# Performance work log

Measured on AMD Instinct MI355X. Metric: run time of the kernel, lower is better.

## Reference

```python
import jax, jax.numpy as jnp
import numpy as np

B, CIN, COUT, H, W, K = 32, 256, 256, 56, 56, 3
STRIDE, PAD, DIL = 1, 1, 1
SPARSITY = 0.9  # fraction of weight entries pruned to zero


def setup_inputs() -> dict:
    key = jax.random.key(0)
    kx, kw, km = jax.random.split(key, 3)
    x = jax.random.normal(kx, (B, CIN, H, W), dtype=jnp.float32)
    w = jax.random.normal(kw, (COUT, CIN, K, K), dtype=jnp.float32)
    mask = (jax.random.uniform(km, (COUT, CIN, K, K)) > SPARSITY).astype(jnp.float32)
    w = w * mask
    return {"x": x, "weight": w}


def reference(x, weight):
    # Faithful math of SparseConv2D.forward (sparse path == nn.Conv2d, bias=None):
    # NCHW input, OIHW weight, stride/pad/dilation as configured.
    out = jax.lax.conv_general_dilated(
        x, weight,
        window_strides=(STRIDE, STRIDE),
        padding=[(PAD, PAD), (PAD, PAD)],
        rhs_dilation=(DIL, DIL),
        dimension_numbers=("NCHW", "OIHW", "NCHW"),
    )
    return out  # [B, COUT, H_out, W_out]
```

## Files before the change

kernel.cpp:

```cpp
#include <hip/hip_runtime.h>


typedef __attribute__((ext_vector_type(8))) short short8;
typedef __attribute__((ext_vector_type(4))) float f32x4;
typedef __attribute__((ext_vector_type(4))) int i32x4;

constexpr int BB = 32, CIN = 256, COUT = 256, H = 56, W = 56, HW = H * W;
constexpr int HP = 58, WP = 58;

constexpr size_t XP_ELEMS = (size_t)BB * HP * WP * CIN;
constexpr size_t WB_ELEMS = (size_t)COUT * 9 * CIN;
constexpr size_t WS_NEEDED = (XP_ELEMS + WB_ELEMS) * 2;

__device__ __forceinline__ ushort f2bf(float f) {
    unsigned x = __float_as_uint(f);
    unsigned r = (x + 0x7FFFu + ((x >> 16) & 1u)) >> 16;
    return (ushort)r;
}


__global__ __launch_bounds__(256)
void prep_xp(const float* __restrict__ x, ushort* __restrict__ xp) {
    const int bi = blockIdx.x;
    const int b = bi / HP, i = bi % HP;
    ushort* dst = xp + (size_t)bi * WP * CIN;
    const int tid = threadIdx.x;

    if (i == 0 || i == HP - 1) {
        i32x4 z = {0, 0, 0, 0};
        for (int k = tid; k < WP * CIN / 8; k += 256) ((i32x4*)dst)[k] = z;
        return;
    }

    __shared__ ushort t[W][CIN + 2];
    const int lane = tid & 63, wv = tid >> 6;
    if (lane < W) {
        const float* src = x + (size_t)b * CIN * HW + (size_t)(i - 1) * W + lane;
        for (int cin = wv; cin < CIN; cin += 4)
            t[lane][cin] = f2bf(src[(size_t)cin * HW]);
    }
    __syncthreads();
    for (int c = 0; c < WP; ++c)
        dst[c * CIN + tid] = (c == 0 || c == WP - 1) ? (ushort)0 : t[c - 1][tid];
}

__global__ __launch_bounds__(256)
void prep_wb2(const float* __restrict__ w, ushort* __restrict__ wb2) {
    const int d = blockIdx.x * 256 + threadIdx.x;
    const int ci = d & 31;
    const int cout = (d >> 5) & 255;
    const int r = d >> 13;
    const int tap = r % 9, cb = r / 9;
    const int cin = cb * 32 + ci;
    wb2[d] = f2bf(w[((size_t)cout * CIN + cin) * 9 + tap]);
}


#define SCHED_FENCE() __builtin_amdgcn_sched_barrier(0)
#define WAITV(N) asm volatile("s_waitcnt vmcnt(" #N ")" ::: "memory")

__device__ __forceinline__ void gload_lds16(const ushort* g, ushort* l) {
    __builtin_amdgcn_global_load_lds(
        (const __attribute__((address_space(1))) void*)g,
        (__attribute__((address_space(3))) void*)l, 16, 0, 0);
}


__global__ __launch_bounds__(512, 4)
void conv_mfma(const ushort* __restrict__ xp, const ushort* __restrict__ wb2,
               float* __restrict__ out) {
    int bx = blockIdx.x;
    bx = (bx & 7) * 112 + (bx >> 3);

    const int b  = bx / 28;
    const int p0 = (bx % 28) * 112;
    const int r0 = p0 / 56;

    const int tid  = threadIdx.x;
    const int wv   = tid >> 6;
    const int lane = tid & 63;
    const int ml   = lane & 15;
    const int g    = lane >> 4;

    __shared__ ushort As[2][1280 * 8];
    __shared__ ushort Xs[2][1280 * 8];
    ushort* dump = &Xs[0][1160 * 8];

    int boff[7];
    #pragma unroll
    for (int nf = 0; nf < 7; ++nf) {
        const int p_  = p0 + nf * 16 + ml;
        const int hl  = (p_ >= p0 + 56) ? 1 : 0;
        const int col = p_ - 56 * (r0 + hl);
        boff[nf] = (hl * 58 + col) * 40 + 8 * g;
    }
    int aoff[2];
    #pragma unroll
    for (int m = 0; m < 2; ++m)
        aoff[m] = (32 * wv + 16 * m + ml) * 40 + 8 * g;

    int goffA[3], goffX[3];
    #pragma unroll
    for (int k = 0; k < 3; ++k) {
        const int c = 512 * k + tid;
        const int s = c / 5, pc = c - s * 5;
        goffA[k] = (c < 1280 && pc < 4) ? s * 32 + pc * 8 : 0;
        goffX[k] = (c < 1160 && pc < 4) ? s * 256 + pc * 8 : 0;
    }
    const size_t xbase = ((size_t)b * HP + r0) * WP * CIN;

    f32x4 acc[2][7] = {};

    #define STAGE_A(T, BUF)                                                     \
        { const ushort* _s = wb2 + (size_t)(T) * 8192;                          \
          _Pragma("unroll")                                                     \
          for (int k = 0; k < 3; ++k) {                                         \
              ushort* _d = (k == 2 && wv >= 4) ? dump                           \
                           : &As[BUF][(512 * k + 64 * wv) * 8];                 \
              gload_lds16(_s + goffA[k], _d);                                   \
          } }
    #define STAGE_X(CB, BUF)                                                    \
        { const ushort* _s = xp + xbase + (CB) * 32;                            \
          _Pragma("unroll")                                                     \
          for (int k = 0; k < 3; ++k) {                                         \
              ushort* _d = (k == 2 && wv >= 4) ? dump                           \
                           : &Xs[BUF][(512 * k + 64 * wv) * 8];                 \
              gload_lds16(_s + goffX[k], _d);                                   \
          } }

    STAGE_A(0, 0);
    STAGE_A(1, 1);
    STAGE_X(0, 0);
    WAITV(0);
    __builtin_amdgcn_s_barrier();

    #pragma unroll
    for (int cb = 0; cb < 8; ++cb) {
        #pragma unroll
        for (int tap = 0; tap < 9; ++tap) {
            const int t = cb * 9 + tap;

            if (t == 71)                            { WAITV(0); }
            else if ((tap == 7 || tap == 8) && cb < 7) { WAITV(6); }
            else                                    { WAITV(3); }
            SCHED_FENCE();
            __builtin_amdgcn_s_barrier();
            SCHED_FENCE();

            const ushort* Ab = &As[t & 1][0];
            const ushort* Xb = &Xs[cb & 1][0];
            const int kh = tap / 3, kw = tap - kh * 3;
            const int toff = (kh * 58 + kw) * 40;

            short8 av[2], bv[7];
            #pragma unroll
            for (int m = 0; m < 2; ++m) av[m] = *(const short8*)(Ab + aoff[m]);
            #pragma unroll
            for (int nf = 0; nf < 7; ++nf) bv[nf] = *(const short8*)(Xb + boff[nf] + toff);

            __builtin_amdgcn_s_setprio(1);
            #pragma unroll
            for (int m = 0; m < 2; ++m)
                #pragma unroll
                for (int nf = 0; nf < 7; ++nf)
                    acc[m][nf] = __builtin_amdgcn_mfma_f32_16x16x32_bf16(
                                     av[m], bv[nf], acc[m][nf], 0, 0, 0);
            __builtin_amdgcn_s_setprio(0);
            SCHED_FENCE();
            __builtin_amdgcn_s_barrier();
            SCHED_FENCE();

            if (t < 70) STAGE_A(t + 2, t & 1);
            if (tap == 7 && cb < 7) STAGE_X(cb + 1, (cb + 1) & 1);
            SCHED_FENCE();
        }
    }

    float* ob = out + (size_t)b * COUT * HW;
    #pragma unroll
    for (int m = 0; m < 2; ++m)
        #pragma unroll
        for (int nf = 0; nf < 7; ++nf)
            #pragma unroll
            for (int r = 0; r < 4; ++r) {
                const int cout_l = 32 * wv + 16 * m + 4 * g + r;
                const int p_ = p0 + 16 * nf + ml;
                ob[(size_t)cout_l * HW + p_] = acc[m][nf][r];
            }
    #undef STAGE_A
    #undef STAGE_X
}


constexpr int WSZ = CIN * 9;
constexpr int NIN = 54 * 54;

__global__ __launch_bounds__(256)
void sparse_conv3x3(const float* __restrict__ x,
                    const float* __restrict__ wgt,
                    float* __restrict__ out) {
    const int bc = blockIdx.x, cout = bc % COUT, b = bc / COUT;
    const int tid = threadIdx.x;
    __shared__ int2 s_ent[WSZ];
    __shared__ unsigned char s_kk[WSZ];
    __shared__ int s_cnt[257];
    const float* wc = wgt + (size_t)cout * WSZ;
    float mv[9]; int cnt = 0;
    #pragma unroll
    for (int i = 0; i < 9; ++i) { mv[i] = wc[tid * 9 + i]; if (mv[i] != 0.0f) cnt++; }
    s_cnt[tid] = cnt; __syncthreads();
    if (tid == 0) { int run = 0; for (int t = 0; t < 256; ++t) { int c = s_cnt[t]; s_cnt[t] = run; run += c; } s_cnt[256] = run; }
    __syncthreads();
    { int pos = s_cnt[tid];
      #pragma unroll
      for (int i = 0; i < 9; ++i) if (mv[i] != 0.0f) {
          const int kh = i / 3, kw = i - kh * 3;
          int2 e; e.x = (tid * HW + (kh - 1) * W + (kw - 1)) * 4; e.y = __float_as_int(mv[i]);
          s_ent[pos] = e; s_kk[pos] = (unsigned char)(kh | (kw << 4)); pos++; } }
    __syncthreads();
    const int nnz = s_cnt[256];
    const char* xb = (const char*)(x + (size_t)b * CIN * HW);
    float* ob = out + (size_t)bc * HW;
    for (int o = tid; o < HW; o += 256) {
        int h, w; bool interior = (o < NIN);
        if (interior) { h = 1 + o / 54; w = 1 + (o - (h - 1) * 54); }
        else { int o2 = o - NIN;
            if (o2 < 56) { h = 0; w = o2; } else if (o2 < 112) { h = 55; w = o2 - 56; }
            else if (o2 < 166) { h = 1 + (o2 - 112); w = 0; } else { h = 1 + (o2 - 166); w = 55; } }
        const char* pb = xb + (size_t)(h * W + w) * 4;
        float acc = 0.0f;
        if (interior) {
            #pragma unroll 4
            for (int e = 0; e < nnz; ++e) { const int2 en = s_ent[e];
                acc = fmaf(__int_as_float(en.y), *(const float*)(pb + en.x), acc); }
        } else {
            const int h1 = h - 1, w1 = w - 1;
            for (int e = 0; e < nnz; ++e) { const int2 en = s_ent[e]; const int kk = s_kk[e];
                const int hh = h1 + (kk & 15), ww = w1 + (kk >> 4);
                if ((unsigned)hh < (unsigned)H && (unsigned)ww < (unsigned)W)
                    acc = fmaf(__int_as_float(en.y), *(const float*)(pb + en.x), acc); } }
        ob[h * W + w] = acc;
    }
}


extern "C" void kernel_launch(void* const* d_in, const int* in_sizes, int n_in,
                              void* d_out, int out_size, void* d_ws, size_t ws_size,
                              hipStream_t stream) {
    const float* x = (const float*)d_in[0];
    const float* w = (const float*)d_in[1];
    float* out = (float*)d_out;

    if (ws_size >= WS_NEEDED) {
        ushort* xp = (ushort*)d_ws;
        ushort* wbp = xp + XP_ELEMS;
        prep_xp<<<BB * HP, 256, 0, stream>>>(x, xp);
        prep_wb2<<<(int)(WB_ELEMS / 256), 256, 0, stream>>>(w, wbp);
        conv_mfma<<<896, 512, 0, stream>>>(xp, wbp, out);
    } else {
        sparse_conv3x3<<<BB * COUT, 256, 0, stream>>>(x, w, out);
    }
}
```

Measured before the change: 162.0 us.

## Halve block threads and give each wave a 64-row cout tile

The conv MFMA kernel now runs 256 threads (4 waves) per block instead of 512 (8 waves). Each wave computes 64 output channels (4x7 MFMA tiles) rather than 32, so every B fragment loaded from LDS feeds more MFMAs. Global-to-LDS staging is rebalanced to 5 loads per thread and the vmcnt waits are retuned to match. The cost is roughly double the accumulator registers per thread and fewer waves per CU to hide latency, which may lower occupancy.

```diff
diff --git a/kernel.cpp b/kernel.cpp
--- a/kernel.cpp
+++ b/kernel.cpp
@@ -66,7 +66,7 @@
 }
 
 
-__global__ __launch_bounds__(512, 4)
+__global__ __launch_bounds__(256, 2)
 void conv_mfma(const ushort* __restrict__ xp, const ushort* __restrict__ wb2,
                float* __restrict__ out) {
     int bx = blockIdx.x;
@@ -84,7 +84,6 @@
 
     __shared__ ushort As[2][1280 * 8];
     __shared__ ushort Xs[2][1280 * 8];
-    ushort* dump = &Xs[0][1160 * 8];
 
     int boff[7];
     #pragma unroll
@@ -94,39 +93,35 @@
         const int col = p_ - 56 * (r0 + hl);
         boff[nf] = (hl * 58 + col) * 40 + 8 * g;
     }
-    int aoff[2];
-    #pragma unroll
-    for (int m = 0; m < 2; ++m)
-        aoff[m] = (32 * wv + 16 * m + ml) * 40 + 8 * g;
-
-    int goffA[3], goffX[3];
-    #pragma unroll
-    for (int k = 0; k < 3; ++k) {
-        const int c = 512 * k + tid;
+    int aoff[4];
+    #pragma unroll
+    for (int mi = 0; mi < 4; ++mi)
+        aoff[mi] = (64 * wv + 16 * mi + ml) * 40 + 8 * g;
+
+    int goffA[5], goffX[5];
+    #pragma unroll
+    for (int k = 0; k < 5; ++k) {
+        const int c = 256 * k + tid;
         const int s = c / 5, pc = c - s * 5;
-        goffA[k] = (c < 1280 && pc < 4) ? s * 32 + pc * 8 : 0;
+        goffA[k] = (pc < 4) ? s * 32 + pc * 8 : 0;
         goffX[k] = (c < 1160 && pc < 4) ? s * 256 + pc * 8 : 0;
     }
     const size_t xbase = ((size_t)b * HP + r0) * WP * CIN;
 
-    f32x4 acc[2][7] = {};
+    f32x4 acc[4][7] = {};
 
     #define STAGE_A(T, BUF)                                                     \
         { const ushort* _s = wb2 + (size_t)(T) * 8192;                          \
           _Pragma("unroll")                                                     \
-          for (int k = 0; k < 3; ++k) {                                         \
-              ushort* _d = (k == 2 && wv >= 4) ? dump                           \
-                           : &As[BUF][(512 * k + 64 * wv) * 8];                 \
-              gload_lds16(_s + goffA[k], _d);                                   \
-          } }
+          for (int k = 0; k < 5; ++k)                                           \
+              gload_lds16(_s + goffA[k], &As[BUF][(256 * k + 64 * wv) * 8]);    \
+        }
     #define STAGE_X(CB, BUF)                                                    \
         { const ushort* _s = xp + xbase + (CB) * 32;                            \
           _Pragma("unroll")                                                     \
-          for (int k = 0; k < 3; ++k) {                                         \
-              ushort* _d = (k == 2 && wv >= 4) ? dump                           \
-                           : &Xs[BUF][(512 * k + 64 * wv) * 8];                 \
-              gload_lds16(_s + goffX[k], _d);                                   \
-          } }
+          for (int k = 0; k < 5; ++k)                                           \
+              gload_lds16(_s + goffX[k], &Xs[BUF][(256 * k + 64 * wv) * 8]);    \
+        }
 
     STAGE_A(0, 0);
     STAGE_A(1, 1);
@@ -140,9 +135,9 @@
         for (int tap = 0; tap < 9; ++tap) {
             const int t = cb * 9 + tap;
 
-            if (t == 71)                            { WAITV(0); }
-            else if ((tap == 7 || tap == 8) && cb < 7) { WAITV(6); }
-            else                                    { WAITV(3); }
+            if (t == 71)                      { WAITV(0); }
+            else if (tap == 8 && cb < 7)      { WAITV(10); }
+            else                              { WAITV(5);  }
             SCHED_FENCE();
             __builtin_amdgcn_s_barrier();
             SCHED_FENCE();
@@ -152,19 +147,19 @@
             const int kh = tap / 3, kw = tap - kh * 3;
             const int toff = (kh * 58 + kw) * 40;
 
-            short8 av[2], bv[7];
-            #pragma unroll
-            for (int m = 0; m < 2; ++m) av[m] = *(const short8*)(Ab + aoff[m]);
+            short8 av[4], bv[7];
+            #pragma unroll
+            for (int mi = 0; mi < 4; ++mi) av[mi] = *(const short8*)(Ab + aoff[mi]);
             #pragma unroll
             for (int nf = 0; nf < 7; ++nf) bv[nf] = *(const short8*)(Xb + boff[nf] + toff);
 
             __builtin_amdgcn_s_setprio(1);
             #pragma unroll
-            for (int m = 0; m < 2; ++m)
+            for (int mi = 0; mi < 4; ++mi)
                 #pragma unroll
                 for (int nf = 0; nf < 7; ++nf)
-                    acc[m][nf] = __builtin_amdgcn_mfma_f32_16x16x32_bf16(
-                                     av[m], bv[nf], acc[m][nf], 0, 0, 0);
+                    acc[mi][nf] = __builtin_amdgcn_mfma_f32_16x16x32_bf16(
+                                      av[mi], bv[nf], acc[mi][nf], 0, 0, 0);
             __builtin_amdgcn_s_setprio(0);
             SCHED_FENCE();
             __builtin_amdgcn_s_barrier();
@@ -178,14 +173,14 @@
 
     float* ob = out + (size_t)b * COUT * HW;
     #pragma unroll
-    for (int m = 0; m < 2; ++m)
+    for (int mi = 0; mi < 4; ++mi)
         #pragma unroll
         for (int nf = 0; nf < 7; ++nf)
             #pragma unroll
             for (int r = 0; r < 4; ++r) {
-                const int cout_l = 32 * wv + 16 * m + 4 * g + r;
+                const int cout_l = 64 * wv + 16 * mi + 4 * g + r;
                 const int p_ = p0 + 16 * nf + ml;
-                ob[(size_t)cout_l * HW + p_] = acc[m][nf][r];
+                ob[(size_t)cout_l * HW + p_] = acc[mi][nf][r];
             }
     #undef STAGE_A
     #undef STAGE_X
@@ -256,7 +251,7 @@
         ushort* wbp = xp + XP_ELEMS;
         prep_xp<<<BB * HP, 256, 0, stream>>>(x, xp);
         prep_wb2<<<(int)(WB_ELEMS / 256), 256, 0, stream>>>(w, wbp);
-        conv_mfma<<<896, 512, 0, stream>>>(xp, wbp, out);
+        conv_mfma<<<896, 256, 0, stream>>>(xp, wbp, out);
     } else {
         sparse_conv3x3<<<BB * COUT, 256, 0, stream>>>(x, w, out);
     }
```

After: 158.2 us. -2.3%, faster.
